# Kernel tuning notes

Measured on AMD Instinct MI355X. Metric: run time of the kernel, lower is better.

The kernel has to match this reference:

```python
import jax, jax.numpy as jnp
import numpy as np

D_MODEL = 1024
N_HEADS = 16
D_HEAD = D_MODEL // N_HEADS
RANK = 128
KNOW_RANK = 128
N_COMPRESS = 64
N_EXPAND = 32
N_KNOW = 16384
TOPK_C = 8
TOPK_E = 4
KNOW_K = 8
B, S = 8, 1024
EPS_LN = 1e-5


def setup_inputs() -> dict:
    key = jax.random.key(0)
    ks = jax.random.split(key, 16)
    inp = {
        'x': jax.random.normal(ks[0], (B, S, D_MODEL), jnp.float32),
        'importance': jax.random.uniform(ks[1], (B, S), jnp.float32),
        # routers, stored as [d_model, n] so out = x @ W
        'Wc': jax.random.normal(ks[2], (D_MODEL, N_COMPRESS), jnp.float32) * 0.02,
        'WQr': jax.random.normal(ks[3], (D_MODEL, N_EXPAND), jnp.float32) * 0.02,
        'WKr': jax.random.normal(ks[4], (D_MODEL, N_EXPAND), jnp.float32) * 0.02,
        'WVr': jax.random.normal(ks[5], (D_MODEL, N_EXPAND), jnp.float32) * 0.02,
        'Wm': jax.random.normal(ks[6], (D_MODEL, N_COMPRESS), jnp.float32) * 0.02,
        # shared neuron pools
        'compress_neurons': jax.random.normal(ks[7], (N_COMPRESS, D_MODEL, RANK), jnp.float32) / np.sqrt(D_MODEL),
        'expand_pool': jax.random.normal(ks[8], (N_EXPAND, RANK, D_MODEL), jnp.float32) / np.sqrt(RANK),
        'knowledge_K': jax.random.normal(ks[9], (N_KNOW, KNOW_RANK), jnp.float32) * 0.02,
        'knowledge_V': jax.random.normal(ks[10], (N_KNOW, D_MODEL), jnp.float32) * 0.02,
        # output projection stored as [d_in, d_out]
        'W_O': jax.random.normal(ks[11], (D_MODEL, D_MODEL), jnp.float32) / np.sqrt(D_MODEL),
        'ln1_s': jnp.ones((D_MODEL,), jnp.float32),
        'ln1_b': jnp.zeros((D_MODEL,), jnp.float32),
        'ln2_s': jnp.ones((D_MODEL,), jnp.float32),
        'ln2_b': jnp.zeros((D_MODEL,), jnp.float32),
    }
    return inp


def _layernorm(x, s, b):
    mu = jnp.mean(x, axis=-1, keepdims=True)
    var = jnp.mean(jnp.square(x - mu), axis=-1, keepdims=True)
    return (x - mu) * jax.lax.rsqrt(var + EPS_LN) * s + b


def _topk_sparsify(w, k):
    # w: [B, n] -> sparse renormalized weights [B, n]
    vals, idx = jax.lax.top_k(w, k)
    rows = jnp.arange(w.shape[0])[:, None]
    sparse = jnp.zeros_like(w).at[rows, idx].set(vals)
    return sparse / (jnp.sum(sparse, axis=-1, keepdims=True) + 1e-8)


def _route(nx, importance, W, k):
    pref = jax.nn.softmax(jnp.einsum('bsd,dn->bsn', nx, W), axis=-1)
    dense = jnp.einsum('bs,bsn->bn', importance, pref)
    return _topk_sparsify(dense, k)


def _forward(x, importance, Wc, WQr, WKr, WVr, Wm, compress_neurons,
             expand_pool, knowledge_K, knowledge_V, W_O, ln1_s, ln1_b, ln2_s, ln2_b):
    Bx, Sx, D = x.shape
    n1 = _layernorm(x, ln1_s, ln1_b)

    # --- attention routing ---
    cw = _route(n1, importance, Wc, TOPK_C)
    ewQ = _route(n1, importance, WQr, TOPK_E)
    ewK = _route(n1, importance, WKr, TOPK_E)
    ewV = _route(n1, importance, WVr, TOPK_E)

    # --- synthesized low-rank attention weights ---
    shared_compress = jnp.einsum('bn,ndr->bdr', cw, compress_neurons)
    h = jnp.einsum('bsd,bdr->bsr', n1, shared_compress)
    EQ = jnp.einsum('bn,nrd->brd', ewQ, expand_pool)
    EK = jnp.einsum('bn,nrd->brd', ewK, expand_pool)
    EV = jnp.einsum('bn,nrd->brd', ewV, expand_pool)
    Q = jnp.einsum('bsr,brd->bsd', h, EQ).reshape(Bx, Sx, N_HEADS, D_HEAD).transpose(0, 2, 1, 3)
    K = jnp.einsum('bsr,brd->bsd', h, EK).reshape(Bx, Sx, N_HEADS, D_HEAD).transpose(0, 2, 1, 3)
    V = jnp.einsum('bsr,brd->bsd', h, EV).reshape(Bx, Sx, N_HEADS, D_HEAD).transpose(0, 2, 1, 3)

    scores = jnp.einsum('bhqd,bhkd->bhqk', Q, K) / np.sqrt(D_HEAD)
    causal = jnp.tril(jnp.ones((Sx, Sx), bool))
    scores = jnp.where(causal, scores, jnp.finfo(scores.dtype).min)
    attn = jax.nn.softmax(scores, axis=-1)
    attn_out = jnp.einsum('bhqk,bhkd->bhqd', attn, V).transpose(0, 2, 1, 3).reshape(Bx, Sx, D)
    attn_out = attn_out @ W_O
    x = x + attn_out

    # --- memory ---
    n2 = _layernorm(x, ln2_s, ln2_b)
    mw = _route(n2, importance, Wm, TOPK_C)
    sc_m = jnp.einsum('bn,ndr->bdr', mw, compress_neurons)
    Qm = jnp.einsum('bsd,bdr->bsr', n2, sc_m)  # knowledge_rank == rank -> no query_proj
    mscores = jnp.einsum('bsr,nr->bsn', Qm, knowledge_K) / np.sqrt(KNOW_RANK)
    topv, topi = jax.lax.top_k(mscores, KNOW_K)
    w = jax.nn.softmax(topv, axis=-1)  # [B,S,k]
    selV = knowledge_V[topi]  # [B,S,k,D]
    mem_out = jnp.einsum('bsk,bskd->bsd', w, selV)
    return x + mem_out


def reference(x, importance, Wc, WQr, WKr, WVr, Wm, compress_neurons,
              expand_pool, knowledge_K, knowledge_V, W_O, ln1_s, ln1_b, ln2_s, ln2_b):
    return _forward(x, importance, Wc, WQr, WKr, WVr, Wm, compress_neurons,
                    expand_pool, knowledge_K, knowledge_V, W_O, ln1_s, ln1_b, ln2_s, ln2_b)
```

## Files before the change

### kernel.cpp

```cpp
#include <hip/hip_runtime.h>
#include <hip/hip_bf16.h>

#define BD 8
#define SD 1024
#define DM 1024
#define NH 16
#define DH 64
#define RK 128
#define NK 16384

typedef __attribute__((ext_vector_type(8))) short bf16x8;
typedef __attribute__((ext_vector_type(4))) float f32x4;

__device__ __forceinline__ unsigned short f2b(float f) {
    unsigned u = __float_as_uint(f);
    unsigned r = (u + 0x7FFFu + ((u >> 16) & 1u)) >> 16;
    return (unsigned short)r;
}
__device__ __forceinline__ float b2f(unsigned short h) {
    return __uint_as_float(((unsigned)h) << 16);
}

__global__ void __launch_bounds__(256) ln_kernel(const float* __restrict__ x,
                                                 const float* __restrict__ sc,
                                                 const float* __restrict__ bi,
                                                 unsigned short* __restrict__ outh,
                                                 unsigned short* __restrict__ outl) {
    const int tok = blockIdx.x;
    __shared__ float xs[DM];
    __shared__ float red[256];
    const float* xp = x + (size_t)tok * DM;
    float s = 0.f;
    for (int i = threadIdx.x; i < DM; i += 256) { float v = xp[i]; xs[i] = v; s += v; }
    red[threadIdx.x] = s; __syncthreads();
    for (int st = 128; st; st >>= 1) { if (threadIdx.x < st) red[threadIdx.x] += red[threadIdx.x + st]; __syncthreads(); }
    float mu = red[0] * (1.f / DM);
    __syncthreads();
    float vs = 0.f;
    for (int i = threadIdx.x; i < DM; i += 256) { float d = xs[i] - mu; vs += d * d; }
    red[threadIdx.x] = vs; __syncthreads();
    for (int st = 128; st; st >>= 1) { if (threadIdx.x < st) red[threadIdx.x] += red[threadIdx.x + st]; __syncthreads(); }
    float rs = rsqrtf(red[0] * (1.f / DM) + 1e-5f);
    for (int i = threadIdx.x; i < DM; i += 256) {
        float v = (xs[i] - mu) * rs * sc[i] + bi[i];
        unsigned short h = f2b(v);
        outh[(size_t)tok * DM + i] = h;
        outl[(size_t)tok * DM + i] = f2b(v - b2f(h));
    }
}

__global__ void __launch_bounds__(256) concatw_kernel(const float* __restrict__ Wc,
                                                      const float* __restrict__ WQr,
                                                      const float* __restrict__ WKr,
                                                      const float* __restrict__ WVr,
                                                      const float* __restrict__ Wm,
                                                      unsigned short* __restrict__ WTh,
                                                      unsigned short* __restrict__ WTl) {
    const int i = blockIdx.x * 256 + threadIdx.x;
    const int c = i >> 10, d = i & 1023;
    float v = 0.f;
    if (c < 64)       v = Wc[d * 64 + c];
    else if (c < 96)  v = WQr[d * 32 + c - 64];
    else if (c < 128) v = WKr[d * 32 + c - 96];
    else if (c < 160) v = WVr[d * 32 + c - 128];
    else if (c >= 192) v = Wm[d * 64 + c - 192];
    unsigned short h = f2b(v);
    WTh[i] = h;
    WTl[i] = f2b(v - b2f(h));
}

__global__ void __launch_bounds__(256) gemm_split(const unsigned short* __restrict__ Ah,
                                                  const unsigned short* __restrict__ Al,
                                                  const unsigned short* __restrict__ Bh,
                                                  const unsigned short* __restrict__ Bl,
                                                  float* __restrict__ C,
                                                  int N, int K) {
    const int row0 = blockIdx.y * 128, col0 = blockIdx.x * 64;
    const int t = threadIdx.x;
    const int w = t >> 6, l = t & 63, lq = l & 15, lg = l >> 4;
    __shared__ unsigned short sAh[128 * 64];
    __shared__ unsigned short sAl[128 * 64];
    __shared__ unsigned short sBh[64 * 64];
    __shared__ unsigned short sBl[64 * 64];
    f32x4 acc[2][4];
    #pragma unroll
    for (int mi = 0; mi < 2; mi++)
        #pragma unroll
        for (int ni = 0; ni < 4; ni++) acc[mi][ni] = f32x4{0.f, 0.f, 0.f, 0.f};

    for (int k0 = 0; k0 < K; k0 += 64) {
        __syncthreads();
        #pragma unroll
        for (int p = 0; p < 4; p++) {
            const int e = t * 8 + p * 2048;
            const int row = e >> 6, col = e & 63;
            const int sw = (e * 2) ^ ((row & 7) << 4);
            *(bf16x8*)((char*)sAh + sw) = *(const bf16x8*)(Ah + (size_t)(row0 + row) * K + k0 + col);
            *(bf16x8*)((char*)sAl + sw) = *(const bf16x8*)(Al + (size_t)(row0 + row) * K + k0 + col);
        }
        #pragma unroll
        for (int p = 0; p < 2; p++) {
            const int e = t * 8 + p * 2048;
            const int row = e >> 6, col = e & 63;
            const int sw = (e * 2) ^ ((row & 7) << 4);
            *(bf16x8*)((char*)sBh + sw) = *(const bf16x8*)(Bh + (size_t)(col0 + row) * K + k0 + col);
            *(bf16x8*)((char*)sBl + sw) = *(const bf16x8*)(Bl + (size_t)(col0 + row) * K + k0 + col);
        }
        __syncthreads();
        #pragma unroll
        for (int kk = 0; kk < 2; kk++) {
            bf16x8 ah[2], al[2], bh[4], bl[4];
            #pragma unroll
            for (int mi = 0; mi < 2; mi++) {
                const int r = w * 32 + mi * 16 + lq;
                const int off = (r * 128 + lg * 16 + kk * 64) ^ ((r & 7) << 4);
                ah[mi] = *(const bf16x8*)((const char*)sAh + off);
                al[mi] = *(const bf16x8*)((const char*)sAl + off);
            }
            #pragma unroll
            for (int ni = 0; ni < 4; ni++) {
                const int r = ni * 16 + lq;
                const int off = (r * 128 + lg * 16 + kk * 64) ^ ((r & 7) << 4);
                bh[ni] = *(const bf16x8*)((const char*)sBh + off);
                bl[ni] = *(const bf16x8*)((const char*)sBl + off);
            }
            #pragma unroll
            for (int mi = 0; mi < 2; mi++)
                #pragma unroll
                for (int ni = 0; ni < 4; ni++) {
                    acc[mi][ni] = __builtin_amdgcn_mfma_f32_16x16x32_bf16(ah[mi], bh[ni], acc[mi][ni], 0, 0, 0);
                    acc[mi][ni] = __builtin_amdgcn_mfma_f32_16x16x32_bf16(ah[mi], bl[ni], acc[mi][ni], 0, 0, 0);
                    acc[mi][ni] = __builtin_amdgcn_mfma_f32_16x16x32_bf16(al[mi], bh[ni], acc[mi][ni], 0, 0, 0);
                }
        }
    }
    #pragma unroll
    for (int mi = 0; mi < 2; mi++)
        #pragma unroll
        for (int j = 0; j < 4; j++) {
            const int row = row0 + w * 32 + mi * 16 + lg * 4 + j;
            #pragma unroll
            for (int ni = 0; ni < 4; ni++)
                C[(size_t)row * N + col0 + ni * 16 + lq] = acc[mi][ni][j];
        }
}

__global__ void __launch_bounds__(256) softpref_kernel(const float* __restrict__ lgt,
                                                       const float* __restrict__ imp,
                                                       float* __restrict__ wpref) {
    const int tok = blockIdx.x * 64 + (threadIdx.x >> 2);
    const int sg = threadIdx.x & 3;
    const int o = (sg == 0) ? 0 : (64 + 32 * (sg - 1));
    const int n = (sg == 0) ? 64 : 32;
    const float* lp = lgt + (size_t)tok * 192 + o;
    float m = -1e30f;
    for (int i = 0; i < n; i++) m = fmaxf(m, lp[i]);
    float ss = 0.f;
    for (int i = 0; i < n; i++) ss += __expf(lp[i] - m);
    const float scl = imp[tok] / ss;
    float* wp = wpref + (size_t)tok * 160 + o;
    for (int i = 0; i < n; i++) wp[i] = __expf(lp[i] - m) * scl;
}

__global__ void __launch_bounds__(256) softm_kernel(const float* __restrict__ lgt,
                                                    const float* __restrict__ imp,
                                                    float* __restrict__ wpref) {
    const int tok = blockIdx.x * 256 + threadIdx.x;
    const float* lp = lgt + (size_t)tok * 64;
    float m = -1e30f;
    for (int i = 0; i < 64; i++) m = fmaxf(m, lp[i]);
    float ss = 0.f;
    for (int i = 0; i < 64; i++) ss += __expf(lp[i] - m);
    const float scl = imp[tok] / ss;
    for (int i = 0; i < 64; i++) wpref[(size_t)tok * 64 + i] = __expf(lp[i] - m) * scl;
}

__global__ void __launch_bounds__(256) reduce_pref(const float* __restrict__ wpref,
                                                   float* __restrict__ dense,
                                                   int ncols, int outoff) {
    const int b = blockIdx.x / ncols, c = blockIdx.x % ncols;
    __shared__ float red[256];
    float s = 0.f;
    for (int si = threadIdx.x; si < SD; si += 256)
        s += wpref[((size_t)(b * SD + si)) * ncols + c];
    red[threadIdx.x] = s; __syncthreads();
    for (int st = 128; st; st >>= 1) { if (threadIdx.x < st) red[threadIdx.x] += red[threadIdx.x + st]; __syncthreads(); }
    if (threadIdx.x == 0) dense[b * 224 + outoff + c] = red[0];
}

__global__ void topk_kernel(const float* __restrict__ dense,
                            int* __restrict__ ridx, float* __restrict__ rw,
                            int r0, int nr) {
    const int t = threadIdx.x;
    if (t >= BD * nr) return;
    const int b = t / nr, r = r0 + (t % nr);
    const int offs[5] = {0, 64, 96, 128, 160};
    const int ns[5]   = {64, 32, 32, 32, 64};
    const int ks[5]   = {8, 4, 4, 4, 8};
    const float* dv = dense + b * 224 + offs[r];
    const int n = ns[r], k = ks[r];
    unsigned long long mask = 0;
    float vals[8]; int idxs[8];
    float ssum = 0.f;
    for (int kk = 0; kk < k; kk++) {
        float best = -1e30f; int bi = 0;
        for (int i = 0; i < n; i++)
            if (!((mask >> i) & 1ull) && dv[i] > best) { best = dv[i]; bi = i; }
        mask |= 1ull << bi;
        vals[kk] = best; idxs[kk] = bi; ssum += best;
    }
    float inv = 1.f / (ssum + 1e-8f);
    for (int kk = 0; kk < 8; kk++) {
        ridx[(b * 5 + r) * 8 + kk] = (kk < k) ? idxs[kk] : 0;
        rw[(b * 5 + r) * 8 + kk]   = (kk < k) ? vals[kk] * inv : 0.f;
    }
}

__global__ void __launch_bounds__(256) combine_t_kernel(const float* __restrict__ pool,
                                                        const int* __restrict__ ridx,
                                                        const float* __restrict__ rw,
                                                        int router, int kc,
                                                        unsigned short* __restrict__ outT,
                                                        int Rp, int Cp, long long sOut) {
    const int b = blockIdx.z;
    const int r0 = blockIdx.y * 64, c0 = blockIdx.x * 64;
    __shared__ float ls[64][65];
    const int* ii = ridx + (b * 5 + router) * 8;
    const float* ww = rw + (b * 5 + router) * 8;
    const int t = threadIdx.x;
    const int rr = t >> 4, cc = (t & 15) * 4;
    #pragma unroll
    for (int p = 0; p < 4; p++) {
        const int r = rr + p * 16;
        float4 acc = {0.f, 0.f, 0.f, 0.f};
        for (int kk = 0; kk < kc; kk++) {
            const float w = ww[kk];
            float4 v = *(const float4*)&pool[((size_t)ii[kk] * Rp + r0 + r) * Cp + c0 + cc];
            acc.x += w * v.x; acc.y += w * v.y; acc.z += w * v.z; acc.w += w * v.w;
        }
        ls[r][cc] = acc.x; ls[r][cc + 1] = acc.y; ls[r][cc + 2] = acc.z; ls[r][cc + 3] = acc.w;
    }
    __syncthreads();
    unsigned short* op = outT + (size_t)b * sOut;
    #pragma unroll
    for (int q = 0; q < 2; q++) {
        const int c = (t >> 3) + q * 32;
        const int r8 = (t & 7) * 8;
        union { unsigned short s[8]; bf16x8 v; } u;
        #pragma unroll
        for (int j = 0; j < 8; j++) u.s[j] = f2b(ls[r8 + j][c]);
        *(bf16x8*)(op + (size_t)(c0 + c) * Rp + r0 + r8) = u.v;
    }
}

__global__ void __launch_bounds__(256) tcvt_kernel(const float* __restrict__ src,
                                                   unsigned short* __restrict__ dst,
                                                   int R, int Cc) {
    __shared__ float ls[64][65];
    const int r0 = blockIdx.y * 64, c0 = blockIdx.x * 64;
    const int t = threadIdx.x;
    #pragma unroll
    for (int p = 0; p < 16; p++) {
        const int e = p * 256 + t;
        const int r = e >> 6, c = e & 63;
        ls[r][c] = src[(size_t)(r0 + r) * Cc + c0 + c];
    }
    __syncthreads();
    #pragma unroll
    for (int p = 0; p < 16; p++) {
        const int e = p * 256 + t;
        const int c = e >> 6, r = e & 63;
        dst[(size_t)(c0 + c) * R + r0 + r] = f2b(ls[r][c]);
    }
}

__global__ void __launch_bounds__(256) cvt_bf16_kernel(const float* __restrict__ src,
                                                       unsigned short* __restrict__ dst,
                                                       float scale, int n4) {
    const int i = blockIdx.x * 256 + threadIdx.x;
    if (i >= n4) return;
    float4 v = ((const float4*)src)[i];
    unsigned r0 = (unsigned)f2b(v.x * scale) | ((unsigned)f2b(v.y * scale) << 16);
    unsigned r1 = (unsigned)f2b(v.z * scale) | ((unsigned)f2b(v.w * scale) << 16);
    uint2 o; o.x = r0; o.y = r1;
    ((uint2*)dst)[i] = o;
}

template<int OUTB, int HASX>
__global__ void __launch_bounds__(256) gemm_bf16(const unsigned short* __restrict__ A,
                                                 const unsigned short* __restrict__ Bt,
                                                 const float* __restrict__ X,
                                                 void* __restrict__ Cv,
                                                 int M, int N, int K,
                                                 long long sA, long long sB, long long sC) {
    const int bz = blockIdx.z;
    const unsigned short* Ab = A + (size_t)bz * sA;
    const unsigned short* Btb = Bt + (size_t)bz * sB;
    const int row0 = blockIdx.y * 128, col0 = blockIdx.x * 128;
    const int t = threadIdx.x;
    const int w = t >> 6, l = t & 63, lq = l & 15, lg = l >> 4;
    const int wr = w >> 1, wc = w & 1;
    __shared__ unsigned short As[128 * 64];
    __shared__ unsigned short Bs[128 * 64];
    f32x4 acc[4][4];
    #pragma unroll
    for (int mi = 0; mi < 4; mi++)
        #pragma unroll
        for (int ni = 0; ni < 4; ni++) acc[mi][ni] = f32x4{0.f, 0.f, 0.f, 0.f};

    for (int k0 = 0; k0 < K; k0 += 64) {
        __syncthreads();
        #pragma unroll
        for (int p = 0; p < 4; p++) {
            const int e = t * 8 + p * 2048;
            const int row = e >> 6, col = e & 63;
            bf16x8 va = *(const bf16x8*)(Ab + (size_t)(row0 + row) * K + k0 + col);
            *(bf16x8*)((char*)As + ((row * 128 + col * 2) ^ ((row & 7) << 4))) = va;
            bf16x8 vb = *(const bf16x8*)(Btb + (size_t)(col0 + row) * K + k0 + col);
            *(bf16x8*)((char*)Bs + ((row * 128 + col * 2) ^ ((row & 7) << 4))) = vb;
        }
        __syncthreads();
        #pragma unroll
        for (int kk = 0; kk < 2; kk++) {
            bf16x8 af[4], bg[4];
            #pragma unroll
            for (int mi = 0; mi < 4; mi++) {
                const int r = wr * 64 + mi * 16 + lq;
                af[mi] = *(const bf16x8*)((const char*)As + ((r * 128 + lg * 16 + kk * 64) ^ ((r & 7) << 4)));
            }
            #pragma unroll
            for (int ni = 0; ni < 4; ni++) {
                const int r = wc * 64 + ni * 16 + lq;
                bg[ni] = *(const bf16x8*)((const char*)Bs + ((r * 128 + lg * 16 + kk * 64) ^ ((r & 7) << 4)));
            }
            #pragma unroll
            for (int mi = 0; mi < 4; mi++)
                #pragma unroll
                for (int ni = 0; ni < 4; ni++)
                    acc[mi][ni] = __builtin_amdgcn_mfma_f32_16x16x32_bf16(af[mi], bg[ni], acc[mi][ni], 0, 0, 0);
        }
    }
    #pragma unroll
    for (int mi = 0; mi < 4; mi++) {
        #pragma unroll
        for (int j = 0; j < 4; j++) {
            const int row = row0 + wr * 64 + mi * 16 + lg * 4 + j;
            #pragma unroll
            for (int ni = 0; ni < 4; ni++) {
                const int col = col0 + wc * 64 + ni * 16 + lq;
                float v = acc[mi][ni][j];
                if (HASX) v += X[(size_t)row * N + col];
                if (OUTB) ((unsigned short*)Cv)[(size_t)bz * sC + (size_t)row * N + col] = f2b(v);
                else      ((float*)Cv)[(size_t)bz * sC + (size_t)row * N + col] = v;
            }
        }
    }
}

__global__ void __launch_bounds__(256) gemm_h(const unsigned short* __restrict__ A,
                                              const unsigned short* __restrict__ Bt,
                                              unsigned short* __restrict__ C,
                                              int K,
                                              long long sA, long long sB, long long sC) {
    const int bz = blockIdx.z;
    const unsigned short* Ab = A + (size_t)bz * sA;
    const unsigned short* Btb = Bt + (size_t)bz * sB;
    const int row0 = blockIdx.y * 64;
    const int t = threadIdx.x;
    const int w = t >> 6, l = t & 63, lq = l & 15, lg = l >> 4;
    __shared__ unsigned short As[64 * 64];
    __shared__ unsigned short Bs[128 * 64];
    f32x4 acc[8];
    #pragma unroll
    for (int ni = 0; ni < 8; ni++) acc[ni] = f32x4{0.f, 0.f, 0.f, 0.f};

    for (int k0 = 0; k0 < K; k0 += 64) {
        __syncthreads();
        #pragma unroll
        for (int p = 0; p < 2; p++) {
            const int e = t * 8 + p * 2048;
            const int row = e >> 6, col = e & 63;
            bf16x8 va = *(const bf16x8*)(Ab + (size_t)(row0 + row) * K + k0 + col);
            *(bf16x8*)((char*)As + ((row * 128 + col * 2) ^ ((row & 7) << 4))) = va;
        }
        #pragma unroll
        for (int p = 0; p < 4; p++) {
            const int e = t * 8 + p * 2048;
            const int row = e >> 6, col = e & 63;
            bf16x8 vb = *(const bf16x8*)(Btb + (size_t)row * K + k0 + col);
            *(bf16x8*)((char*)Bs + ((row * 128 + col * 2) ^ ((row & 7) << 4))) = vb;
        }
        __syncthreads();
        #pragma unroll
        for (int kk = 0; kk < 2; kk++) {
            const int ra = w * 16 + lq;
            bf16x8 af = *(const bf16x8*)((const char*)As + ((ra * 128 + lg * 16 + kk * 64) ^ ((ra & 7) << 4)));
            #pragma unroll
            for (int ni = 0; ni < 8; ni++) {
                const int r = ni * 16 + lq;
                bf16x8 bg = *(const bf16x8*)((const char*)Bs + ((r * 128 + lg * 16 + kk * 64) ^ ((r & 7) << 4)));
                acc[ni] = __builtin_amdgcn_mfma_f32_16x16x32_bf16(af, bg, acc[ni], 0, 0, 0);
            }
        }
    }
    #pragma unroll
    for (int j = 0; j < 4; j++) {
        const int row = row0 + w * 16 + lg * 4 + j;
        #pragma unroll
        for (int ni = 0; ni < 8; ni++)
            C[(size_t)bz * sC + (size_t)row * 128 + ni * 16 + lq] = f2b(acc[ni][j]);
    }
}

#define SWZV(d) (((((d) >> 1) ^ ((d) >> 3)) & 7) << 4)
__global__ void __launch_bounds__(256) attn_mfma_kernel(const unsigned short* __restrict__ Q,
                                                        const unsigned short* __restrict__ K,
                                                        const unsigned short* __restrict__ V,
                                                        unsigned short* __restrict__ O,
                                                        int ldq) {
    const int qt = blockIdx.x, hh = blockIdx.y, b = blockIdx.z;
    const int t = threadIdx.x;
    const int w = t >> 6, l = t & 63, lq = l & 15, lg = l >> 4;

    __shared__ unsigned short ks[2][64 * 64];
    __shared__ unsigned short vt[2][64 * 64];
    __shared__ unsigned short pl[4][16 * 64];

    const size_t base = (size_t)b * SD * ldq + (size_t)hh * DH;
    const size_t obase = (size_t)b * SD * DM + (size_t)hh * DH;
    const int qA = qt;
    const int qB = 15 - qt;

    bf16x8 aqA[2], aqB[2];
    {
        const unsigned short* qp = Q + base + (size_t)(qA * 64 + w * 16 + lq) * ldq + lg * 8;
        aqA[0] = *(const bf16x8*)qp; aqA[1] = *(const bf16x8*)(qp + 32);
        const unsigned short* qp2 = Q + base + (size_t)(qB * 64 + w * 16 + lq) * ldq + lg * 8;
        aqB[0] = *(const bf16x8*)qp2; aqB[1] = *(const bf16x8*)(qp2 + 32);
    }

    f32x4 oA[4], oB[4];
    #pragma unroll
    for (int dt = 0; dt < 4; dt++) { oA[dt] = f32x4{0.f,0.f,0.f,0.f}; oB[dt] = f32x4{0.f,0.f,0.f,0.f}; }
    float mA[4] = {-1e30f,-1e30f,-1e30f,-1e30f}, sA[4] = {0.f,0.f,0.f,0.f};
    float mB[4] = {-1e30f,-1e30f,-1e30f,-1e30f}, sB[4] = {0.f,0.f,0.f,0.f};

    const int ntile = 16 - qt;
    const int srow = t >> 3;
    const int scol = (t & 7) * 8;

    int cur = 0;

    #pragma unroll
    for (int p = 0; p < 2; p++) {
        const int row = srow + 32 * p;
        bf16x8 kv = *(const bf16x8*)(K + base + (size_t)row * ldq + scol);
        *(bf16x8*)((char*)&ks[0][0] + ((row * 128 + scol * 2) ^ ((row & 7) << 4))) = kv;
        bf16x8 vv = *(const bf16x8*)(V + base + (size_t)row * ldq + scol);
        #pragma unroll
        for (int j2 = 0; j2 < 8; j2++) {
            const int d = scol + j2;
            *(unsigned short*)((char*)&vt[0][0] + ((d * 128 + row * 2) ^ SWZV(d))) = (unsigned short)vv[j2];
        }
    }
    __syncthreads();

    auto compute = [&](int q0, const bf16x8* aq, f32x4* o_, float* m_, float* s_, int kt) {
        const f32x4 zero4 = {0.f, 0.f, 0.f, 0.f};
        f32x4 sacc[4];
        #pragma unroll
        for (int ct = 0; ct < 4; ct++) {
            const int krow = ct * 16 + lq;
            bf16x8 b0 = *(const bf16x8*)((const char*)&ks[cur][0] + ((krow * 128 + lg * 16) ^ ((lq & 7) << 4)));
            bf16x8 b1 = *(const bf16x8*)((const char*)&ks[cur][0] + ((krow * 128 + lg * 16 + 64) ^ ((lq & 7) << 4)));
            f32x4 s = __builtin_amdgcn_mfma_f32_16x16x32_bf16(aq[0], b0, zero4, 0, 0, 0);
            s = __builtin_amdgcn_mfma_f32_16x16x32_bf16(aq[1], b1, s, 0, 0, 0);
            sacc[ct] = s;
        }
        float tm[4];
        #pragma unroll
        for (int j = 0; j < 4; j++) {
            const int qg = q0 * 64 + w * 16 + lg * 4 + j;
            float mx = -1e30f;
            #pragma unroll
            for (int ct = 0; ct < 4; ct++) {
                const int kg = kt * 64 + ct * 16 + lq;
                float v = sacc[ct][j] * 0.125f;
                v = (kg <= qg) ? v : -1e30f;
                sacc[ct][j] = v;
                mx = fmaxf(mx, v);
            }
            #pragma unroll
            for (int d = 1; d < 16; d <<= 1) mx = fmaxf(mx, __shfl_xor(mx, d));
            tm[j] = mx;
        }
        #pragma unroll
        for (int j = 0; j < 4; j++) {
            const float nm = fmaxf(m_[j], tm[j]);
            const float so = __expf(m_[j] - nm);
            m_[j] = nm;
            float rs = 0.f;
            const int prow = lg * 4 + j;
            #pragma unroll
            for (int ct = 0; ct < 4; ct++) {
                const float p = __expf(sacc[ct][j] - nm);
                rs += p;
                const int byteoff = ((prow * 128) + (ct * 16 + lq) * 2) ^ ((prow & 7) << 4);
                *(unsigned short*)((char*)&pl[w][0] + byteoff) = f2b(p);
            }
            #pragma unroll
            for (int d = 1; d < 16; d <<= 1) rs += __shfl_xor(rs, d);
            s_[j] = s_[j] * so + rs;
            #pragma unroll
            for (int dt = 0; dt < 4; dt++) o_[dt][j] *= so;
        }
        asm volatile("s_waitcnt lgkmcnt(0)" ::: "memory");
        __builtin_amdgcn_sched_barrier(0);
        #pragma unroll
        for (int c = 0; c < 2; c++) {
            bf16x8 pa = *(const bf16x8*)((const char*)&pl[w][0] +
                          ((lq * 128 + lg * 16 + 64 * c) ^ ((lq & 7) << 4)));
            #pragma unroll
            for (int dt = 0; dt < 4; dt++) {
                const int dd = dt * 16 + lq;
                bf16x8 bv = *(const bf16x8*)((const char*)&vt[cur][0] +
                              ((dd * 128 + lg * 16 + 64 * c) ^ SWZV(dd)));
                o_[dt] = __builtin_amdgcn_mfma_f32_16x16x32_bf16(pa, bv, o_[dt], 0, 0, 0);
            }
        }
    };

    const int mymaxA = qA * 64 + w * 16 + 15;
    for (int kt = 0; kt < ntile; kt++) {
        bf16x8 kN[2], vN[2];
        const bool pre = (kt + 1 < ntile);
        if (pre) {
            #pragma unroll
            for (int p = 0; p < 2; p++) {
                const int row = srow + 32 * p;
                kN[p] = *(const bf16x8*)(K + base + (size_t)((kt + 1) * 64 + row) * ldq + scol);
                vN[p] = *(const bf16x8*)(V + base + (size_t)((kt + 1) * 64 + row) * ldq + scol);
            }
        }
        compute(qB, aqB, oB, mB, sB, kt);
        if (kt * 64 <= mymaxA) compute(qA, aqA, oA, mA, sA, kt);
        if (pre) {
            #pragma unroll
            for (int p = 0; p < 2; p++) {
                const int row = srow + 32 * p;
                *(bf16x8*)((char*)&ks[cur ^ 1][0] + ((row * 128 + scol * 2) ^ ((row & 7) << 4))) = kN[p];
                #pragma unroll
                for (int j2 = 0; j2 < 8; j2++) {
                    const int d = scol + j2;
                    *(unsigned short*)((char*)&vt[cur ^ 1][0] + ((d * 128 + row * 2) ^ SWZV(d))) =
                        (unsigned short)vN[p][j2];
                }
            }
        }
        __syncthreads();
        cur ^= 1;
    }

    #pragma unroll
    for (int j = 0; j < 4; j++) {
        const float invA = 1.f / sA[j];
        const float invB = 1.f / sB[j];
        const int rowA = qA * 64 + w * 16 + lg * 4 + j;
        const int rowB = qB * 64 + w * 16 + lg * 4 + j;
        unsigned short* opA = O + obase + (size_t)rowA * DM;
        unsigned short* opB = O + obase + (size_t)rowB * DM;
        #pragma unroll
        for (int dt = 0; dt < 4; dt++) {
            opA[dt * 16 + lq] = f2b(oA[dt][j] * invA);
            opB[dt * 16 + lq] = f2b(oB[dt][j] * invB);
        }
    }
}
#undef SWZV

#define CE(a, b) { float hi_ = fmaxf(a, b), lo_ = fminf(a, b); a = hi_; b = lo_; }
__global__ void __launch_bounds__(512, 4) know_score_kernel(const unsigned short* __restrict__ Qmb,
                                                            const unsigned short* __restrict__ kKb,
                                                            float* __restrict__ cand) {
    const int t = threadIdx.x;
    const int w = t >> 6, l = t & 63, lq = l & 15, lg = l >> 4;
    const int tok0 = blockIdx.x * 16;
    __shared__ unsigned short ks[8][16 * 128];

    bf16x8 aq[4];
    {
        const unsigned short* qp = Qmb + (size_t)(tok0 + lq) * 128 + lg * 8;
        #pragma unroll
        for (int c = 0; c < 4; c++) aq[c] = *(const bf16x8*)(qp + c * 32);
    }

    float L[4][8];
    #pragma unroll
    for (int j = 0; j < 4; j++)
        #pragma unroll
        for (int s = 0; s < 8; s++) L[j][s] = __uint_as_float(0xF2000000u | (unsigned)s);

    const unsigned short* gsrc = kKb + (((size_t)w * 2048) << 7) + l * 8;
    unsigned short* myks = &ks[w][0];

    bf16x8 vreg[4];
    #pragma unroll
    for (int p = 0; p < 4; p++) vreg[p] = *(const bf16x8*)(gsrc + p * 512);

    for (int t4 = 0; t4 < 32; t4++) {
        float B[4][4];
        #pragma unroll
        for (int sub = 0; sub < 4; sub++) {
            const int kt = t4 * 4 + sub;
            #pragma unroll
            for (int p = 0; p < 4; p++) {
                const int e = p * 512 + l * 8;
                const int row = e >> 7;
                *(bf16x8*)((char*)myks + ((e * 2) ^ ((row & 7) << 4))) = vreg[p];
            }
            if (kt < 127) {
                const unsigned short* src2 = gsrc + (size_t)(kt + 1) * 2048;
                #pragma unroll
                for (int p = 0; p < 4; p++) vreg[p] = *(const bf16x8*)(src2 + p * 512);
            }
            {
                const char* kb = (const char*)myks + lq * 256;
                const int sw = (lq & 7) << 4;
                f32x4 s = {0.f, 0.f, 0.f, 0.f};
                #pragma unroll
                for (int c = 0; c < 4; c++) {
                    bf16x8 bv = *(const bf16x8*)(kb + ((c * 64 + lg * 16) ^ sw));
                    s = __builtin_amdgcn_mfma_f32_16x16x32_bf16(aq[c], bv, s, 0, 0, 0);
                }
                const unsigned keyb = (unsigned)(w * 2048 + kt * 16 + lq);
                #pragma unroll
                for (int j = 0; j < 4; j++) {
                    unsigned u = __float_as_uint(s[j]);
                    B[j][sub] = __uint_as_float((u & 0xFFFFC000u) | keyb);
                }
            }
        }
        #pragma unroll
        for (int j = 0; j < 4; j++) {
            CE(B[j][0], B[j][2]); CE(B[j][1], B[j][3]);
            CE(B[j][0], B[j][1]); CE(B[j][2], B[j][3]);
            CE(B[j][1], B[j][2]);
            L[j][4] = fmaxf(L[j][4], B[j][3]);
            L[j][5] = fmaxf(L[j][5], B[j][2]);
            L[j][6] = fmaxf(L[j][6], B[j][1]);
            L[j][7] = fmaxf(L[j][7], B[j][0]);
            CE(L[j][0], L[j][4]); CE(L[j][1], L[j][5]); CE(L[j][2], L[j][6]); CE(L[j][3], L[j][7]);
            CE(L[j][0], L[j][2]); CE(L[j][1], L[j][3]); CE(L[j][4], L[j][6]); CE(L[j][5], L[j][7]);
            CE(L[j][0], L[j][1]); CE(L[j][2], L[j][3]); CE(L[j][4], L[j][5]); CE(L[j][6], L[j][7]);
        }
    }
    #pragma unroll
    for (int j = 0; j < 4; j++) {
        const int tok = tok0 + lg * 4 + j;
        float* cp = cand + ((size_t)tok << 10) + w * 128 + lq * 8;
        #pragma unroll
        for (int ss = 0; ss < 8; ss++) cp[ss] = L[j][ss];
    }
}
#undef CE

__global__ void __launch_bounds__(256) know_out_kernel(const float* __restrict__ cand,
                                                       const float* __restrict__ kV,
                                                       float* __restrict__ out) {
    const int t = threadIdx.x, w = t >> 6, l = t & 63;
    const int tok = blockIdx.x * 4 + w;
    const float* cp = cand + ((size_t)tok << 10);
    float lv[16];
    #pragma unroll
    for (int i = 0; i < 16; i++) lv[i] = cp[i * 64 + l];

    float topv[8]; int topi[8];
    #pragma unroll
    for (int kk = 0; kk < 8; kk++) {
        float m = lv[0];
        #pragma unroll
        for (int i = 1; i < 16; i++) m = fmaxf(m, lv[i]);
        #pragma unroll
        for (int d = 1; d < 64; d <<= 1) m = fmaxf(m, __shfl_xor(m, d));
        topv[kk] = m;
        topi[kk] = (int)(__float_as_uint(m) & 0x3FFFu);
        #pragma unroll
        for (int i = 0; i < 16; i++) lv[i] = (lv[i] == m) ? -1e31f : lv[i];
    }
    const float mx = topv[0];
    float e[8]; float ssum = 0.f;
    #pragma unroll
    for (int kk = 0; kk < 8; kk++) { e[kk] = __expf(topv[kk] - mx); ssum += e[kk]; }
    const float inv = 1.f / ssum;

    float4 acc[4];
    #pragma unroll
    for (int ch = 0; ch < 4; ch++) acc[ch] = float4{0.f, 0.f, 0.f, 0.f};
    #pragma unroll
    for (int kk = 0; kk < 8; kk++) {
        const float wk = e[kk] * inv;
        const float* vp = kV + ((size_t)topi[kk] << 10);
        #pragma unroll
        for (int ch = 0; ch < 4; ch++) {
            float4 v = *(const float4*)(vp + ch * 256 + l * 4);
            acc[ch].x += wk * v.x; acc[ch].y += wk * v.y;
            acc[ch].z += wk * v.z; acc[ch].w += wk * v.w;
        }
    }
    float* op = out + ((size_t)tok << 10);
    #pragma unroll
    for (int ch = 0; ch < 4; ch++) {
        float4 o = *(const float4*)(op + ch * 256 + l * 4);
        o.x += acc[ch].x; o.y += acc[ch].y; o.z += acc[ch].z; o.w += acc[ch].w;
        *(float4*)(op + ch * 256 + l * 4) = o;
    }
}

extern "C" void kernel_launch(void* const* d_in, const int* in_sizes, int n_in,
                              void* d_out, int out_size, void* d_ws, size_t ws_size,
                              hipStream_t stream) {
    const float* x    = (const float*)d_in[0];
    const float* imp  = (const float*)d_in[1];
    const float* Wc   = (const float*)d_in[2];
    const float* WQr  = (const float*)d_in[3];
    const float* WKr  = (const float*)d_in[4];
    const float* WVr  = (const float*)d_in[5];
    const float* Wm   = (const float*)d_in[6];
    const float* cneu = (const float*)d_in[7];
    const float* epool= (const float*)d_in[8];
    const float* kK   = (const float*)d_in[9];
    const float* kV   = (const float*)d_in[10];
    const float* WO   = (const float*)d_in[11];
    const float* ln1s = (const float*)d_in[12];
    const float* ln1b = (const float*)d_in[13];
    const float* ln2s = (const float*)d_in[14];
    const float* ln2b = (const float*)d_in[15];
    float* out = (float*)d_out;

    float* ws = (float*)d_ws;
    size_t o = 0;
    unsigned short* n1h = (unsigned short*)(ws + o); o += (size_t)BD * SD * DM / 2;
    unsigned short* n1l = (unsigned short*)(ws + o); o += (size_t)BD * SD * DM / 2;
    float* lgt   = ws + o; o += (size_t)BD * SD * 192;
    float* wpref = ws + o; o += (size_t)BD * SD * 160;
    float* dense = ws + o; o += (size_t)BD * 224;
    int*   ridx  = (int*)(ws + o); o += (size_t)BD * 5 * 8;
    float* rw    = ws + o; o += (size_t)BD * 5 * 8;
    unsigned short* WTh = (unsigned short*)(ws + o); o += (size_t)256 * 1024 / 2;
    unsigned short* WTl = (unsigned short*)(ws + o); o += (size_t)256 * 1024 / 2;
    unsigned short* scompT = (unsigned short*)(ws + o); o += (size_t)BD * RK * DM / 2;
    unsigned short* E3t = (unsigned short*)(ws + o); o += (size_t)BD * 3 * DM * RK / 2;
    unsigned short* hb  = (unsigned short*)(ws + o); o += (size_t)BD * SD * RK / 2;
    unsigned short* QKV16 = (unsigned short*)(ws + o); o += (size_t)BD * SD * 3072 / 2;
    unsigned short* attnb = (unsigned short*)(ws + o); o += (size_t)BD * SD * DM / 2;
    unsigned short* WOt = (unsigned short*)(ws + o); o += (size_t)DM * DM / 2;
    unsigned short* kKb = (unsigned short*)(ws + o); o += (size_t)NK * RK / 2;
    unsigned short* Qmb = (unsigned short*)(ws + o); o += (size_t)BD * SD * RK / 2;
    float* cand = ws + o; o += (size_t)BD * SD * 1024;

    const int NTOK = BD * SD;
    const long long sE3 = (long long)3 * DM * RK;

    concatw_kernel<<<1024, 256, 0, stream>>>(Wc, WQr, WKr, WVr, Wm, WTh, WTl);
    tcvt_kernel<<<dim3(16, 16, 1), 256, 0, stream>>>(WO, WOt, DM, DM);
    cvt_bf16_kernel<<<(NK * RK / 4) / 256, 256, 0, stream>>>(kK, kKb, 0.0883883476483184f, NK * RK / 4);

    ln_kernel<<<NTOK, 256, 0, stream>>>(x, ln1s, ln1b, n1h, n1l);
    gemm_split<<<dim3(3, NTOK / 128), 256, 0, stream>>>(n1h, n1l, WTh, WTl, lgt, 192, DM);
    softpref_kernel<<<NTOK / 64, 256, 0, stream>>>(lgt, imp, wpref);
    reduce_pref<<<BD * 160, 256, 0, stream>>>(wpref, dense, 160, 0);
    topk_kernel<<<1, 64, 0, stream>>>(dense, ridx, rw, 0, 4);
    combine_t_kernel<<<dim3(2, 16, BD), 256, 0, stream>>>(cneu, ridx, rw, 0, 8, scompT, DM, RK,
        (long long)DM * RK);
    combine_t_kernel<<<dim3(16, 2, BD), 256, 0, stream>>>(epool, ridx, rw, 1, 4,
        E3t + (size_t)0 * DM * RK, RK, DM, sE3);
    combine_t_kernel<<<dim3(16, 2, BD), 256, 0, stream>>>(epool, ridx, rw, 2, 4,
        E3t + (size_t)1 * DM * RK, RK, DM, sE3);
    combine_t_kernel<<<dim3(16, 2, BD), 256, 0, stream>>>(epool, ridx, rw, 3, 4,
        E3t + (size_t)2 * DM * RK, RK, DM, sE3);
    gemm_h<<<dim3(1, SD / 64, BD), 256, 0, stream>>>(n1h, scompT, hb,
        DM, (long long)SD * DM, (long long)RK * DM, (long long)SD * RK);
    gemm_bf16<1, 0><<<dim3(24, 8, BD), 256, 0, stream>>>(hb, E3t, nullptr, QKV16,
        SD, 3072, RK, (long long)SD * RK, sE3, (long long)SD * 3072);
    attn_mfma_kernel<<<dim3(8, NH, BD), 256, 0, stream>>>(QKV16, QKV16 + 1024, QKV16 + 2048,
        attnb, 3072);
    gemm_bf16<0, 1><<<dim3(8, 64, 1), 256, 0, stream>>>(attnb, WOt, x, out,
        NTOK, DM, DM, 0, 0, 0);

    ln_kernel<<<NTOK, 256, 0, stream>>>(out, ln2s, ln2b, n1h, n1l);
    gemm_split<<<dim3(1, NTOK / 128), 256, 0, stream>>>(n1h, n1l,
        WTh + (size_t)192 * 1024, WTl + (size_t)192 * 1024, lgt, 64, DM);
    softm_kernel<<<NTOK / 256, 256, 0, stream>>>(lgt, imp, wpref);
    reduce_pref<<<BD * 64, 256, 0, stream>>>(wpref, dense, 64, 160);
    topk_kernel<<<1, 64, 0, stream>>>(dense, ridx, rw, 4, 1);
    combine_t_kernel<<<dim3(2, 16, BD), 256, 0, stream>>>(cneu, ridx, rw, 4, 8, scompT, DM, RK,
        (long long)DM * RK);
    gemm_h<<<dim3(1, SD / 64, BD), 256, 0, stream>>>(n1h, scompT, Qmb,
        DM, (long long)SD * DM, (long long)RK * DM, (long long)SD * RK);
    know_score_kernel<<<NTOK / 16, 512, 0, stream>>>(Qmb, kKb, cand);
    know_out_kernel<<<NTOK / 4, 256, 0, stream>>>(cand, kV, out);
}
```

Measured before the change: 676.0 us.

## Fuse router softmax with reduction, merge expand combines, shrink knowledge candidate buffer

Router softmax now reduces in shared memory per 64-token chunk and writes only small partial sums, which topk finishes. This removes the large wpref buffer and the separate reduce_pref launch. The three expand-pool combine launches become one kernel with a 24-slice grid, and the attention MFMA sections are wrapped in s_setprio raises. The knowledge scoring kernel merges candidate lists across lanes with shuffle-based bitonic max steps, so it writes 64 candidates per token instead of 1024 and shrinks the work in know_out; the trade-off is extra shuffle work and a serial topk-side sum over 16 partials.

```diff
diff --git a/kernel.cpp b/kernel.cpp
--- a/kernel.cpp
+++ b/kernel.cpp
@@ -145,11 +145,14 @@
         }
 }
 
-__global__ void __launch_bounds__(256) softpref_kernel(const float* __restrict__ lgt,
-                                                       const float* __restrict__ imp,
-                                                       float* __restrict__ wpref) {
-    const int tok = blockIdx.x * 64 + (threadIdx.x >> 2);
-    const int sg = threadIdx.x & 3;
+__global__ void __launch_bounds__(256) softpref_red(const float* __restrict__ lgt,
+                                                    const float* __restrict__ imp,
+                                                    float* __restrict__ partial) {
+    const int b = blockIdx.x, chunk = blockIdx.y;
+    __shared__ float wp[64][161];
+    const int t = threadIdx.x;
+    const int tl = t >> 2, sg = t & 3;
+    const int tok = b * SD + chunk * 64 + tl;
     const int o = (sg == 0) ? 0 : (64 + 32 * (sg - 1));
     const int n = (sg == 0) ? 64 : 32;
     const float* lp = lgt + (size_t)tok * 192 + o;
@@ -158,54 +161,62 @@
     float ss = 0.f;
     for (int i = 0; i < n; i++) ss += __expf(lp[i] - m);
     const float scl = imp[tok] / ss;
-    float* wp = wpref + (size_t)tok * 160 + o;
-    for (int i = 0; i < n; i++) wp[i] = __expf(lp[i] - m) * scl;
-}
-
-__global__ void __launch_bounds__(256) softm_kernel(const float* __restrict__ lgt,
-                                                    const float* __restrict__ imp,
-                                                    float* __restrict__ wpref) {
-    const int tok = blockIdx.x * 256 + threadIdx.x;
-    const float* lp = lgt + (size_t)tok * 64;
-    float m = -1e30f;
-    for (int i = 0; i < 64; i++) m = fmaxf(m, lp[i]);
-    float ss = 0.f;
-    for (int i = 0; i < 64; i++) ss += __expf(lp[i] - m);
-    const float scl = imp[tok] / ss;
-    for (int i = 0; i < 64; i++) wpref[(size_t)tok * 64 + i] = __expf(lp[i] - m) * scl;
-}
-
-__global__ void __launch_bounds__(256) reduce_pref(const float* __restrict__ wpref,
-                                                   float* __restrict__ dense,
-                                                   int ncols, int outoff) {
-    const int b = blockIdx.x / ncols, c = blockIdx.x % ncols;
-    __shared__ float red[256];
-    float s = 0.f;
-    for (int si = threadIdx.x; si < SD; si += 256)
-        s += wpref[((size_t)(b * SD + si)) * ncols + c];
-    red[threadIdx.x] = s; __syncthreads();
-    for (int st = 128; st; st >>= 1) { if (threadIdx.x < st) red[threadIdx.x] += red[threadIdx.x + st]; __syncthreads(); }
-    if (threadIdx.x == 0) dense[b * 224 + outoff + c] = red[0];
-}
-
-__global__ void topk_kernel(const float* __restrict__ dense,
+    for (int i = 0; i < n; i++) wp[tl][o + i] = __expf(lp[i] - m) * scl;
+    __syncthreads();
+    if (t < 160) {
+        float s = 0.f;
+        for (int k = 0; k < 64; k++) s += wp[k][t];
+        partial[((size_t)(b * 16 + chunk)) * 224 + t] = s;
+    }
+}
+
+__global__ void __launch_bounds__(256) softm_red(const float* __restrict__ lgt,
+                                                 const float* __restrict__ imp,
+                                                 float* __restrict__ partial) {
+    const int b = blockIdx.x, chunk = blockIdx.y;
+    __shared__ float wp[64][65];
+    const int t = threadIdx.x;
+    if (t < 64) {
+        const int tok = b * SD + chunk * 64 + t;
+        const float* lp = lgt + (size_t)tok * 64;
+        float m = -1e30f;
+        for (int i = 0; i < 64; i++) m = fmaxf(m, lp[i]);
+        float ss = 0.f;
+        for (int i = 0; i < 64; i++) ss += __expf(lp[i] - m);
+        const float scl = imp[tok] / ss;
+        for (int i = 0; i < 64; i++) wp[t][i] = __expf(lp[i] - m) * scl;
+    }
+    __syncthreads();
+    if (t < 64) {
+        float s = 0.f;
+        for (int k = 0; k < 64; k++) s += wp[k][t];
+        partial[((size_t)(b * 16 + chunk)) * 224 + 160 + t] = s;
+    }
+}
+
+__global__ void topk_kernel(const float* __restrict__ partial,
                             int* __restrict__ ridx, float* __restrict__ rw,
                             int r0, int nr) {
+    __shared__ float dv[40][65];
     const int t = threadIdx.x;
     if (t >= BD * nr) return;
     const int b = t / nr, r = r0 + (t % nr);
     const int offs[5] = {0, 64, 96, 128, 160};
     const int ns[5]   = {64, 32, 32, 32, 64};
     const int ks[5]   = {8, 4, 4, 4, 8};
-    const float* dv = dense + b * 224 + offs[r];
-    const int n = ns[r], k = ks[r];
+    const int n = ns[r], k = ks[r], off = offs[r];
+    for (int i = 0; i < n; i++) {
+        float s = 0.f;
+        for (int c = 0; c < 16; c++) s += partial[((size_t)(b * 16 + c)) * 224 + off + i];
+        dv[t][i] = s;
+    }
     unsigned long long mask = 0;
     float vals[8]; int idxs[8];
     float ssum = 0.f;
     for (int kk = 0; kk < k; kk++) {
         float best = -1e30f; int bi = 0;
         for (int i = 0; i < n; i++)
-            if (!((mask >> i) & 1ull) && dv[i] > best) { best = dv[i]; bi = i; }
+            if (!((mask >> i) & 1ull) && dv[t][i] > best) { best = dv[t][i]; bi = i; }
         mask |= 1ull << bi;
         vals[kk] = best; idxs[kk] = bi; ssum += best;
     }
@@ -253,6 +264,43 @@
     }
 }
 
+__global__ void __launch_bounds__(256) combine_e_kernel(const float* __restrict__ pool,
+                                                        const int* __restrict__ ridx,
+                                                        const float* __restrict__ rw,
+                                                        unsigned short* __restrict__ E3t) {
+    const int z = blockIdx.z;
+    const int b = z & 7, router = 1 + (z >> 3);
+    const int r0 = blockIdx.y * 64, c0 = blockIdx.x * 64;
+    __shared__ float ls[64][65];
+    const int* ii = ridx + (b * 5 + router) * 8;
+    const float* ww = rw + (b * 5 + router) * 8;
+    const int t = threadIdx.x;
+    const int rr = t >> 4, cc = (t & 15) * 4;
+    #pragma unroll
+    for (int p = 0; p < 4; p++) {
+        const int r = rr + p * 16;
+        float4 acc = {0.f, 0.f, 0.f, 0.f};
+        #pragma unroll
+        for (int kk = 0; kk < 4; kk++) {
+            const float w = ww[kk];
+            float4 v = *(const float4*)&pool[((size_t)ii[kk] * RK + r0 + r) * DM + c0 + cc];
+            acc.x += w * v.x; acc.y += w * v.y; acc.z += w * v.z; acc.w += w * v.w;
+        }
+        ls[r][cc] = acc.x; ls[r][cc + 1] = acc.y; ls[r][cc + 2] = acc.z; ls[r][cc + 3] = acc.w;
+    }
+    __syncthreads();
+    unsigned short* op = E3t + (size_t)b * 3 * DM * RK + (size_t)(router - 1) * DM * RK;
+    #pragma unroll
+    for (int q = 0; q < 2; q++) {
+        const int c = (t >> 3) + q * 32;
+        const int r8 = (t & 7) * 8;
+        union { unsigned short s[8]; bf16x8 v; } u;
+        #pragma unroll
+        for (int j = 0; j < 8; j++) u.s[j] = f2b(ls[r8 + j][c]);
+        *(bf16x8*)(op + (size_t)(c0 + c) * RK + r0 + r8) = u.v;
+    }
+}
+
 __global__ void __launch_bounds__(256) tcvt_kernel(const float* __restrict__ src,
                                                    unsigned short* __restrict__ dst,
                                                    int R, int Cc) {
@@ -468,6 +516,7 @@
     auto compute = [&](int q0, const bf16x8* aq, f32x4* o_, float* m_, float* s_, int kt) {
         const f32x4 zero4 = {0.f, 0.f, 0.f, 0.f};
         f32x4 sacc[4];
+        __builtin_amdgcn_s_setprio(1);
         #pragma unroll
         for (int ct = 0; ct < 4; ct++) {
             const int krow = ct * 16 + lq;
@@ -477,6 +526,7 @@
             s = __builtin_amdgcn_mfma_f32_16x16x32_bf16(aq[1], b1, s, 0, 0, 0);
             sacc[ct] = s;
         }
+        __builtin_amdgcn_s_setprio(0);
         float tm[4];
         #pragma unroll
         for (int j = 0; j < 4; j++) {
@@ -516,6 +566,7 @@
         }
         asm volatile("s_waitcnt lgkmcnt(0)" ::: "memory");
         __builtin_amdgcn_sched_barrier(0);
+        __builtin_amdgcn_s_setprio(1);
         #pragma unroll
         for (int c = 0; c < 2; c++) {
             bf16x8 pa = *(const bf16x8*)((const char*)&pl[w][0] +
@@ -528,6 +579,7 @@
                 o_[dt] = __builtin_amdgcn_mfma_f32_16x16x32_bf16(pa, bv, o_[dt], 0, 0, 0);
             }
         }
+        __builtin_amdgcn_s_setprio(0);
     };
 
     const int mymaxA = qA * 64 + w * 16 + 15;
@@ -656,10 +708,32 @@
     }
     #pragma unroll
     for (int j = 0; j < 4; j++) {
-        const int tok = tok0 + lg * 4 + j;
-        float* cp = cand + ((size_t)tok << 10) + w * 128 + lq * 8;
-        #pragma unroll
-        for (int ss = 0; ss < 8; ss++) cp[ss] = L[j][ss];
+        #pragma unroll
+        for (int d = 1; d < 16; d <<= 1) {
+            float P[8];
+            #pragma unroll
+            for (int s = 0; s < 8; s++) P[s] = __shfl_xor(L[j][s], d);
+            L[j][0] = fmaxf(L[j][0], P[7]);
+            L[j][1] = fmaxf(L[j][1], P[6]);
+            L[j][2] = fmaxf(L[j][2], P[5]);
+            L[j][3] = fmaxf(L[j][3], P[4]);
+            L[j][4] = fmaxf(L[j][4], P[3]);
+            L[j][5] = fmaxf(L[j][5], P[2]);
+            L[j][6] = fmaxf(L[j][6], P[1]);
+            L[j][7] = fmaxf(L[j][7], P[0]);
+            CE(L[j][0], L[j][4]); CE(L[j][1], L[j][5]); CE(L[j][2], L[j][6]); CE(L[j][3], L[j][7]);
+            CE(L[j][0], L[j][2]); CE(L[j][1], L[j][3]); CE(L[j][4], L[j][6]); CE(L[j][5], L[j][7]);
+            CE(L[j][0], L[j][1]); CE(L[j][2], L[j][3]); CE(L[j][4], L[j][5]); CE(L[j][6], L[j][7]);
+        }
+    }
+    if (lq == 0) {
+        #pragma unroll
+        for (int j = 0; j < 4; j++) {
+            const int tok = tok0 + lg * 4 + j;
+            float* cp = cand + (size_t)tok * 64 + w * 8;
+            #pragma unroll
+            for (int ss = 0; ss < 8; ss++) cp[ss] = L[j][ss];
+        }
     }
 }
 #undef CE
@@ -669,23 +743,17 @@
                                                        float* __restrict__ out) {
     const int t = threadIdx.x, w = t >> 6, l = t & 63;
     const int tok = blockIdx.x * 4 + w;
-    const float* cp = cand + ((size_t)tok << 10);
-    float lv[16];
-    #pragma unroll
-    for (int i = 0; i < 16; i++) lv[i] = cp[i * 64 + l];
+    float lv = cand[(size_t)tok * 64 + l];
 
     float topv[8]; int topi[8];
     #pragma unroll
     for (int kk = 0; kk < 8; kk++) {
-        float m = lv[0];
-        #pragma unroll
-        for (int i = 1; i < 16; i++) m = fmaxf(m, lv[i]);
+        float m = lv;
         #pragma unroll
         for (int d = 1; d < 64; d <<= 1) m = fmaxf(m, __shfl_xor(m, d));
         topv[kk] = m;
         topi[kk] = (int)(__float_as_uint(m) & 0x3FFFu);
-        #pragma unroll
-        for (int i = 0; i < 16; i++) lv[i] = (lv[i] == m) ? -1e31f : lv[i];
+        lv = (lv == m) ? -1e31f : lv;
     }
     const float mx = topv[0];
     float e[8]; float ssum = 0.f;
@@ -742,8 +810,7 @@
     unsigned short* n1h = (unsigned short*)(ws + o); o += (size_t)BD * SD * DM / 2;
     unsigned short* n1l = (unsigned short*)(ws + o); o += (size_t)BD * SD * DM / 2;
     float* lgt   = ws + o; o += (size_t)BD * SD * 192;
-    float* wpref = ws + o; o += (size_t)BD * SD * 160;
-    float* dense = ws + o; o += (size_t)BD * 224;
+    float* partial = ws + o; o += (size_t)BD * 16 * 224;
     int*   ridx  = (int*)(ws + o); o += (size_t)BD * 5 * 8;
     float* rw    = ws + o; o += (size_t)BD * 5 * 8;
     unsigned short* WTh = (unsigned short*)(ws + o); o += (size_t)256 * 1024 / 2;
@@ -756,7 +823,7 @@
     unsigned short* WOt = (unsigned short*)(ws + o); o += (size_t)DM * DM / 2;
     unsigned short* kKb = (unsigned short*)(ws + o); o += (size_t)NK * RK / 2;
     unsigned short* Qmb = (unsigned short*)(ws + o); o += (size_t)BD * SD * RK / 2;
-    float* cand = ws + o; o += (size_t)BD * SD * 1024;
+    float* cand = ws + o; o += (size_t)BD * SD * 64;
 
     const int NTOK = BD * SD;
     const long long sE3 = (long long)3 * DM * RK;
@@ -767,17 +834,11 @@
 
     ln_kernel<<<NTOK, 256, 0, stream>>>(x, ln1s, ln1b, n1h, n1l);
     gemm_split<<<dim3(3, NTOK / 128), 256, 0, stream>>>(n1h, n1l, WTh, WTl, lgt, 192, DM);
-    softpref_kernel<<<NTOK / 64, 256, 0, stream>>>(lgt, imp, wpref);
-    reduce_pref<<<BD * 160, 256, 0, stream>>>(wpref, dense, 160, 0);
-    topk_kernel<<<1, 64, 0, stream>>>(dense, ridx, rw, 0, 4);
+    softpref_red<<<dim3(BD, 16), 256, 0, stream>>>(lgt, imp, partial);
+    topk_kernel<<<1, 64, 0, stream>>>(partial, ridx, rw, 0, 4);
     combine_t_kernel<<<dim3(2, 16, BD), 256, 0, stream>>>(cneu, ridx, rw, 0, 8, scompT, DM, RK,
         (long long)DM * RK);
-    combine_t_kernel<<<dim3(16, 2, BD), 256, 0, stream>>>(epool, ridx, rw, 1, 4,
-        E3t + (size_t)0 * DM * RK, RK, DM, sE3);
-    combine_t_kernel<<<dim3(16, 2, BD), 256, 0, stream>>>(epool, ridx, rw, 2, 4,
-        E3t + (size_t)1 * DM * RK, RK, DM, sE3);
-    combine_t_kernel<<<dim3(16, 2, BD), 256, 0, stream>>>(epool, ridx, rw, 3, 4,
-        E3t + (size_t)2 * DM * RK, RK, DM, sE3);
+    combine_e_kernel<<<dim3(16, 2, 24), 256, 0, stream>>>(epool, ridx, rw, E3t);
     gemm_h<<<dim3(1, SD / 64, BD), 256, 0, stream>>>(n1h, scompT, hb,
         DM, (long long)SD * DM, (long long)RK * DM, (long long)SD * RK);
     gemm_bf16<1, 0><<<dim3(24, 8, BD), 256, 0, stream>>>(hb, E3t, nullptr, QKV16,
@@ -790,9 +851,8 @@
     ln_kernel<<<NTOK, 256, 0, stream>>>(out, ln2s, ln2b, n1h, n1l);
     gemm_split<<<dim3(1, NTOK / 128), 256, 0, stream>>>(n1h, n1l,
         WTh + (size_t)192 * 1024, WTl + (size_t)192 * 1024, lgt, 64, DM);
-    softm_kernel<<<NTOK / 256, 256, 0, stream>>>(lgt, imp, wpref);
-    reduce_pref<<<BD * 64, 256, 0, stream>>>(wpref, dense, 64, 160);
-    topk_kernel<<<1, 64, 0, stream>>>(dense, ridx, rw, 4, 1);
+    softm_red<<<dim3(BD, 16), 256, 0, stream>>>(lgt, imp, partial);
+    topk_kernel<<<1, 64, 0, stream>>>(partial, ridx, rw, 4, 1);
     combine_t_kernel<<<dim3(2, 16, BD), 256, 0, stream>>>(cneu, ridx, rw, 4, 8, scompT, DM, RK,
         (long long)DM * RK);
     gemm_h<<<dim3(1, SD / 64, BD), 256, 0, stream>>>(n1h, scompT, Qmb,
```

Result: faster. 625.4 us (-7.5%).
